# Performance work log

Measured on AMD Instinct MI355X. Metric: run time of the kernel, lower is better.

Reference implementation:

```python
import jax, jax.numpy as jnp
import numpy as np

THRESH = 1.0
TAU_M = 20.0
TAU_S = 5.0
NUM_STEPS = 8
SCALE = 0.2
BATCH = 8
DM = np.float32(np.exp(-1.0 / TAU_M))
DS = np.float32(np.exp(-1.0 / TAU_S))


@jax.custom_vjp
def spike_fn(x):
    return (x > 0.0).astype(x.dtype)

def _sf_fwd(x):
    return (x > 0.0).astype(x.dtype), x

def _sf_bwd(x, g):
    # rectangular surrogate gradient (lens = 0.5), standard for NOSO/SNN training
    return (g * (jnp.abs(x) < 0.5).astype(x.dtype),)

spike_fn.defvjp(_sf_fwd, _sf_bwd)


def conv5x5(x, w):
    return jax.lax.conv_general_dilated(x, w, (1, 1), ((2, 2), (2, 2)),
                                        dimension_numbers=('NCHW', 'OIHW', 'NCHW'))


def noso_conv(w, in_sp, sav, vm, vs):
    # dual-exponential NOSO neuron: pre-synaptic traces vm/vs, membrane u = sav*(conv(vm)-conv(vs))
    vm = DM * vm + in_sp
    vs = DS * vs + in_sp
    um = conv5x5(vm, w)
    us = conv5x5(vs, w)
    u = sav * (um - us)
    sp = spike_fn(u - THRESH)
    sav = sav * (1.0 - sp)  # one spike per neuron
    return sav, vm, vs, um, u, sp


def noso_fc(w, in_sp, sav, vm, vs):
    vm = DM * vm + in_sp
    vs = DS * vs + in_sp
    um = jnp.einsum('bi,oi->bo', vm, w)
    us = jnp.einsum('bi,oi->bo', vs, w)
    u = sav * (um - us)
    sp = spike_fn(u - THRESH)
    sav = sav * (1.0 - sp)
    return sav, vm, vs, um, u, sp


def minpool(sp, lat):
    # latency-based 2x2 min-pool: pass through the spike whose neuron fired earliest
    b, c, h, w = sp.shape
    s = sp.reshape(b, c, h // 2, 2, w // 2, 2).transpose(0, 1, 2, 4, 3, 5).reshape(b, c, h // 2, w // 2, 4)
    l = lat.reshape(b, c, h // 2, 2, w // 2, 2).transpose(0, 1, 2, 4, 3, 5).reshape(b, c, h // 2, w // 2, 4)
    idx = jnp.argmin(l, axis=-1)
    return jnp.take_along_axis(s, idx[..., None], axis=-1)[..., 0]


def xavier(key, shape, fan_in, fan_out):
    a = np.float32(np.sqrt(6.0 / (fan_in + fan_out)))
    return jax.random.uniform(key, shape, jnp.float32, -a, a)


def setup_inputs():
    key = jax.random.key(0)
    ks = jax.random.split(key, 9)
    inp = {'input': jax.random.uniform(ks[0], (BATCH, 3, 32, 32), jnp.float32)}
    def cw(k, o, i):
        return xavier(k, (o, i, 5, 5), i * 25, o * 25)
    def lw(k, o, i):
        return xavier(k, (o, i), i, o)
    inp['wc1'] = cw(ks[1], 64, 3)
    inp['wc2'] = cw(ks[2], 128, 64)
    inp['wc3'] = cw(ks[3], 256, 128)
    inp['wc4'] = cw(ks[4], 512, 256)
    inp['wc5'] = cw(ks[5], 256, 512)
    inp['wf1'] = lw(ks[6], 1024, 16384)
    inp['wf2'] = lw(ks[7], 512, 1024)
    inp['wf3'] = lw(ks[8], 10, 512)
    inp['batch_size'] = BATCH
    return inp


def forward(input, wc1, wc2, wc3, wc4, wc5, wf1, wf2, wf3, batch_size):
    B = batch_size
    f32 = jnp.float32
    def Z(*s):
        return jnp.zeros((B,) + s, f32)
    def O(*s):
        return jnp.ones((B,) + s, f32)
    carry = {
        'in_u': Z(3, 32, 32),
        'h1': (O(64, 32, 32), Z(3, 32, 32), Z(3, 32, 32)),
        'h2': (O(128, 32, 32), Z(64, 32, 32), Z(64, 32, 32)),
        'h3': (O(256, 16, 16), Z(128, 16, 16), Z(128, 16, 16)),
        'h4': (O(512, 8, 8), Z(256, 8, 8), Z(256, 8, 8)),
        'h5': (O(256, 8, 8), Z(512, 8, 8), Z(512, 8, 8)),
        'f1': (O(1024), Z(16384), Z(16384)),
        'f2': (O(512), Z(1024), Z(1024)),
        'f3': (O(10), Z(512), Z(512)),
        'p1e': Z(128, 32, 32),
        'p1l': float(NUM_STEPS) * O(128, 32, 32),
        'p2e': Z(256, 16, 16),
        'p2l': float(NUM_STEPS) * O(256, 16, 16),
        'te': Z(10),
        'out_t': float(NUM_STEPS) * O(10),
        'out_u': Z(10),
        'sum_sp': jnp.zeros((9,), f32),
    }

    def step(c, _):
        # input encoding neuron (thresh=1, leaky integrate + reset on spike)
        in_u = DM * c['in_u'] + input * SCALE
        in_sp = spike_fn(in_u - 1.0)
        in_u = in_u * (1.0 - in_sp)
        s1, vm1, vs1, um1, u1, sp1 = noso_conv(wc1, in_sp, *c['h1'])
        s2, vm2, vs2, um2, u2, sp2 = noso_conv(wc2, sp1, *c['h2'])
        p1e = c['p1e'] + ((c['p1e'] + (um2 != 0).astype(f32)) != 0).astype(f32)
        p1l = c['p1l'] + jax.lax.stop_gradient(sp2) * (p1e - NUM_STEPS + 1.0)
        s3, vm3, vs3, um3, u3, sp3 = noso_conv(wc3, minpool(sp2, p1l), *c['h3'])
        p2e = c['p2e'] + ((c['p2e'] + (um3 != 0).astype(f32)) != 0).astype(f32)
        p2l = c['p2l'] + jax.lax.stop_gradient(sp3) * (p2e - NUM_STEPS + 1.0)
        s4, vm4, vs4, um4, u4, sp4 = noso_conv(wc4, minpool(sp3, p2l), *c['h4'])
        s5, vm5, vs5, um5, u5, sp5 = noso_conv(wc5, sp4, *c['h5'])
        sf1, vmf1, vsf1, umf1, uf1, spf1 = noso_fc(wf1, sp5.reshape(B, -1), *c['f1'])
        sf2, vmf2, vsf2, umf2, uf2, spf2 = noso_fc(wf2, spf1, *c['f2'])
        sf3, vmf3, vsf3, umf3, uf3, spf3 = noso_fc(wf3, spf2, *c['f3'])
        te = c['te'] + ((c['te'] + (uf3 != 0).astype(f32)) != 0).astype(f32)
        out_t = c['out_t'] + spf3 * jax.lax.stop_gradient(te - NUM_STEPS)  # dodt forward
        out_u = c['out_u'] + spf3 * uf3
        sum_sp = c['sum_sp'] + jnp.stack([in_sp.sum(), sp1.sum(), sp2.sum(), sp3.sum(),
                                          sp4.sum(), sp5.sum(), spf1.sum(), spf2.sum(), spf3.sum()])
        nc = {'in_u': in_u,
              'h1': (s1, vm1, vs1), 'h2': (s2, vm2, vs2), 'h3': (s3, vm3, vs3),
              'h4': (s4, vm4, vs4), 'h5': (s5, vm5, vs5),
              'f1': (sf1, vmf1, vsf1), 'f2': (sf2, vmf2, vsf2), 'f3': (sf3, vmf3, vsf3),
              'p1e': p1e, 'p1l': p1l, 'p2e': p2e, 'p2l': p2l,
              'te': te, 'out_t': out_t, 'out_u': out_u, 'sum_sp': sum_sp}
        return nc, None

    c, _ = jax.lax.scan(step, carry, None, length=NUM_STEPS)
    return c['out_t'], c['out_u'], c['sum_sp']


def reference(input, wc1, wc2, wc3, wc4, wc5, wf1, wf2, wf3, batch_size):
    return forward(input, wc1, wc2, wc3, wc4, wc5, wf1, wf2, wf3, batch_size)
```

## Files before the change

kernel.cpp:

```cpp
#include <hip/hip_runtime.h>
#include <cstddef>

#define B 8
constexpr int TAIL_NB = 256;

constexpr float DM = 0.95122942450071400910f;
constexpr float DS = 0.81873075307798185867f;

constexpr int BS_L0 = 3 * 32 * 32;
constexpr int BS_L1 = 64 * 32 * 32;
constexpr int BS_P1 = 128 * 16 * 16;
constexpr int BS_P2 = 256 * 8 * 8;
constexpr int BS_L4 = 512 * 8 * 8;
constexpr int BS_L5 = 256 * 8 * 8;
constexpr int BS_F1 = 1024;
constexpr int BS_F2 = 512;

constexpr size_t I_L0 = 0;
constexpr size_t I_L1 = I_L0 + 8 * (size_t)B * BS_L0;
constexpr size_t I_P1 = I_L1 + 8 * (size_t)B * BS_L1;
constexpr size_t I_P2 = I_P1 + 8 * (size_t)B * BS_P1;
constexpr size_t I_L4 = I_P2 + 8 * (size_t)B * BS_P2;
constexpr size_t I_L5 = I_L4 + 8 * (size_t)B * BS_L4;
constexpr size_t I_F1 = I_L5 + 8 * (size_t)B * BS_L5;
constexpr size_t I_F2 = I_F1 + 8 * (size_t)B * BS_F1;
constexpr size_t I_CNT = I_F2 + 8 * (size_t)B * BS_F2;
constexpr size_t I_SUMP = I_CNT + 512;
constexpr size_t I_BAR = I_SUMP + 16;
constexpr size_t INT_TOTAL = I_BAR + 2;
constexpr size_t WS_NEED = INT_TOTAL * sizeof(int);

constexpr int ilog2(int n) { int l = 0; while (n > 1) { n >>= 1; ++l; } return l; }

__device__ __forceinline__ int ldcnt(const int* p) {
  return __hip_atomic_load(p, __ATOMIC_RELAXED, __HIP_MEMORY_SCOPE_AGENT);
}

__device__ __forceinline__ void block_stage(bool sp, int idx, int* s_list, int* s_n) {
  unsigned long long bal = __ballot(sp);
  if (bal == 0ull) return;
  int lane = threadIdx.x & 63;
  int leader = (int)__ffsll((unsigned long long)bal) - 1;
  int base = 0;
  if (lane == leader) base = atomicAdd(s_n, __popcll(bal));
  base = __shfl(base, leader);
  if (sp) s_list[base + __popcll(bal & ((1ull << lane) - 1ull))] = idx;
}

__device__ __forceinline__ void wave_append(bool sp, int idx, int* cnt, int* list) {
  unsigned long long bal = __ballot(sp);
  if (bal == 0ull) return;
  int lane = threadIdx.x & 63;
  int leader = (int)__ffsll((unsigned long long)bal) - 1;
  int base = 0;
  if (lane == leader) base = atomicAdd(cnt, __popcll(bal));
  base = __shfl(base, leader);
  if (sp) list[base + __popcll(bal & ((1ull << lane) - 1ull))] = idx;
}

__device__ __forceinline__ bool layer_any(const int* cnt, int ci, int tid, int* s_gate) {
  __syncthreads();
  if (tid == 0) *s_gate = 0;
  __syncthreads();
  if (tid < 64) {
    int t = tid >> 3, b = tid & 7;
    if (ldcnt(cnt + (t * 8 + ci) * 8 + b) > 0) *s_gate = 1;
  }
  __syncthreads();
  return *s_gate != 0;
}

__device__ __forceinline__ void gbar(int* bar, int tid) {
  __threadfence();
  __syncthreads();
  if (tid == 0) {
    int g = __hip_atomic_load(bar + 1, __ATOMIC_RELAXED, __HIP_MEMORY_SCOPE_AGENT);
    int a = __hip_atomic_fetch_add(bar, 1, __ATOMIC_ACQ_REL, __HIP_MEMORY_SCOPE_AGENT);
    if (a == TAIL_NB - 1) {
      __hip_atomic_store(bar, 0, __ATOMIC_RELAXED, __HIP_MEMORY_SCOPE_AGENT);
      __hip_atomic_store(bar + 1, g + 1, __ATOMIC_RELEASE, __HIP_MEMORY_SCOPE_AGENT);
    } else {
      while (__hip_atomic_load(bar + 1, __ATOMIC_ACQUIRE, __HIP_MEMORY_SCOPE_AGENT) == g)
        __builtin_amdgcn_s_sleep(1);
    }
  }
  __syncthreads();
  __threadfence();
}

__global__ __launch_bounds__(512) void k_encode(const float* __restrict__ in,
                                                int* __restrict__ iws) {
  const int tid = threadIdx.x;
  const int b = blockIdx.x;
  int* cnt = iws + I_CNT;
  if (tid < 56) {
    int t = tid / 7, ci = 1 + tid % 7;
    cnt[(t * 8 + ci) * 8 + b] = 0;
  }
  if (b == 0 && tid >= 64 && tid < 82) iws[I_SUMP + (tid - 64)] = 0;
  __shared__ unsigned long long s_bal[8 * 48];
  __shared__ int s_off[8 * 48];
  const int lane = tid & 63, w = tid >> 6;
  float x[6], u[6];
#pragma unroll
  for (int k = 0; k < 6; ++k) {
    x[k] = in[b * BS_L0 + tid + k * 512] * 0.2f;
    u[k] = 0.0f;
  }
  unsigned long long spmall = 0ull;
#pragma clang loop unroll(disable)
  for (int t = 0; t < 8; ++t) {
#pragma unroll
    for (int k = 0; k < 6; ++k) {
      u[k] = DM * u[k] + x[k];
      bool sp = (u[k] - 1.0f > 0.0f);
      if (sp) { u[k] = 0.0f; spmall |= 1ull << (t * 6 + k); }
      unsigned long long bal = __ballot(sp);
      if (lane == 0) s_bal[t * 48 + k * 8 + w] = bal;
    }
  }
  __syncthreads();
  if (lane < 48) {
    const int t = w;
    int v = __popcll(s_bal[t * 48 + lane]);
    int incl = v;
#pragma unroll
    for (int d = 1; d < 64; d <<= 1) {
      int o = __shfl_up(incl, d);
      if (lane >= d) incl += o;
    }
    s_off[t * 48 + lane] = incl - v;
    if (lane == 47) cnt[(t * 8 + 0) * 8 + b] = incl;
  }
  __syncthreads();
#pragma clang loop unroll(disable)
  for (int t = 0; t < 8; ++t) {
    int* list = iws + I_L0 + ((size_t)t * B + b) * BS_L0;
#pragma unroll
    for (int k = 0; k < 6; ++k) {
      if (spmall & (1ull << (t * 6 + k))) {
        int word = k * 8 + w;
        int rank = __popcll(s_bal[t * 48 + word] & ((1ull << lane) - 1ull));
        list[s_off[t * 48 + word] + rank] = tid + k * 512;
      }
    }
  }
}

__global__ __launch_bounds__(1024) void k_conv1(const float* __restrict__ w,
                                                int* __restrict__ iws) {
  const int tid = threadIdx.x;
  const int plane = blockIdx.x;
  const int b = plane >> 6;
  const int oc = plane & 63;
  int* cnt = iws + I_CNT;
  __shared__ float s_acc[8 * 1024];
  __shared__ float s_w[75];
  __shared__ int s_cnt[8];
  if (tid < 8) s_cnt[tid] = ldcnt(cnt + (tid * 8 + 0) * 8 + b);
  if (tid >= 64 && tid < 139) s_w[tid - 64] = w[oc * 75 + (tid - 64)];
#pragma unroll
  for (int t = 0; t < 8; ++t) s_acc[t * 1024 + tid] = 0.0f;
  __syncthreads();
#pragma clang loop unroll(disable)
  for (int t = 0; t < 8; ++t) {
    const int S = s_cnt[t];
    if (S == 0) continue;
    const int* glist = iws + I_L0 + ((size_t)t * B + b) * BS_L0;
    const int total = S << 5;
#pragma clang loop unroll(disable)
    for (int i = tid; i < total; i += 1024) {
      int k = i & 31;
      if (k < 25) {
        int loc = glist[i >> 5];
        int c = loc >> 10;
        int p = loc & 1023;
        int ki = (k * 205) >> 10;
        int oy = (p >> 5) + 2 - ki;
        int ox = (p & 31) + 2 - (k - ki * 5);
        if ((unsigned)oy < 32u && (unsigned)ox < 32u)
          atomicAdd(&s_acc[t * 1024 + (oy << 5) + ox], s_w[c * 25 + k]);
      }
    }
  }
  __syncthreads();
  float um = 0.0f, us = 0.0f, sav = 1.0f;
#pragma clang loop unroll(disable)
  for (int t = 0; t < 8; ++t) {
    float cv = s_acc[t * 1024 + tid];
    float m = DM * um + cv;
    float s2 = DS * us + cv;
    um = m;
    us = s2;
    float uu = sav * (m - s2);
    bool sp = (uu - 1.0f > 0.0f);
    if (sp) sav = 0.0f;
    wave_append(sp, (oc << 10) + tid, cnt + (t * 8 + 1) * 8 + b,
                iws + I_L1 + ((size_t)t * B + b) * BS_L1);
  }
}

template <int CIN, int COUT, int H, int W, bool POOL, int PPB, bool WLDS>
__device__ void conv_phase(int bid, int tid, const float* __restrict__ w, int* cnt, int in_ci,
                           int out_ci, const int* __restrict__ in_list0, int in_bs,
                           int* __restrict__ out_list0, int out_bs, float* sump_layer,
                           float* s_acc, float* s_plb, float* s_spb, float* s_w, int* s_list,
                           int* s_n, int* s_base, int* s_uc, int* s_cnt) {
  constexpr int HW = H * W;
  constexpr int HWlog = ilog2(HW);
  constexpr int Wlog = ilog2(W);
  constexpr int PPT = (HW + 255) / 256;
  int wcount = 0;
  const int b = (bid * PPB) >> ilog2(COUT);
  if (tid < 8) s_cnt[tid] = ldcnt(cnt + (tid * 8 + in_ci) * 8 + b);
  __syncthreads();
#pragma clang loop unroll(disable)
  for (int pl = 0; pl < PPB; ++pl) {
    const int plane = bid * PPB + pl;
    const int oc = plane & (COUT - 1);
    if constexpr (WLDS) {
#pragma clang loop unroll(disable)
      for (int j = tid; j < CIN * 25; j += 256) s_w[j] = w[(size_t)oc * CIN * 25 + j];
    }
    float um[PPT], us[PPT], sav[PPT], pe[PPT], plat[PPT];
#pragma unroll
    for (int k = 0; k < PPT; ++k) {
      um[k] = 0.0f; us[k] = 0.0f; sav[k] = 1.0f; pe[k] = 0.0f; plat[k] = 8.0f;
    }
    bool active = false;
#pragma clang loop unroll(disable)
    for (int t = 0; t < 8; ++t) {
      const int S = s_cnt[t];
      if (!active && S == 0) continue;
      active = true;
#pragma clang loop unroll(disable)
      for (int p = tid; p < HW; p += 256) s_acc[p] = 0.0f;
      if (tid == 0) *s_n = 0;
      __syncthreads();
      const int* list = in_list0 + ((size_t)t * B + b) * in_bs;
#pragma clang loop unroll(disable)
      for (int s = tid; s < S; s += 256) {
        int loc = list[s];
        int c = loc >> HWlog;
        int p = loc & (HW - 1);
        int y = p >> Wlog, x = p & (W - 1);
        const float* wp = WLDS ? (const float*)s_w + c * 25 : w + ((size_t)oc * CIN + c) * 25;
#pragma clang loop unroll(disable)
        for (int ki = 0; ki < 5; ++ki) {
          int oy = y + 2 - ki;
          if ((unsigned)oy < (unsigned)H) {
#pragma clang loop unroll(disable)
            for (int kj = 0; kj < 5; ++kj) {
              int ox = x + 2 - kj;
              if ((unsigned)ox < (unsigned)W) atomicAdd(&s_acc[oy * W + ox], wp[ki * 5 + kj]);
            }
          }
        }
      }
      __syncthreads();
#pragma unroll
      for (int k = 0; k < PPT; ++k) {
        int p = tid + k * 256;
        bool lane_ok = (p < HW);
        float cv = lane_ok ? s_acc[p] : 0.0f;
        float m = DM * um[k] + cv;
        float s2 = DS * us[k] + cv;
        um[k] = m;
        us[k] = s2;
        float uu = sav[k] * (m - s2);
        bool sp = lane_ok && (uu - 1.0f > 0.0f);
        if (sp) sav[k] = 0.0f;
        if constexpr (POOL) {
          unsigned long long bal = __ballot(sp);
          if ((tid & 63) == 0) wcount += (int)__popcll(bal);
          if (lane_ok) {
            float act = (m != 0.0f) ? 1.0f : 0.0f;
            float pen = pe[k] + (((pe[k] + act) != 0.0f) ? 1.0f : 0.0f);
            pe[k] = pen;
            if (sp) plat[k] += pen - 7.0f;
            s_plb[p] = plat[k];
            s_spb[p] = sp ? 1.0f : 0.0f;
          }
        } else {
          block_stage(sp, (oc << HWlog) + p, s_list, s_n);
        }
      }
      __syncthreads();
      if constexpr (POOL) {
        constexpr int HP = H / 2, WP = W / 2;
#pragma clang loop unroll(disable)
        for (int q = tid; q < HP * WP; q += 256) {
          int py = q / WP, px = q - py * WP;
          int base = (2 * py) * W + 2 * px;
          float l0 = s_plb[base], l1 = s_plb[base + 1], l2 = s_plb[base + W],
                l3 = s_plb[base + W + 1];
          int off = 0;
          float lm = l0;
          if (l1 < lm) { lm = l1; off = 1; }
          if (l2 < lm) { lm = l2; off = W; }
          if (l3 < lm) { lm = l3; off = W + 1; }
          bool psp = (s_spb[base + off] != 0.0f);
          block_stage(psp, oc * (HP * WP) + q, s_list, s_n);
        }
        __syncthreads();
      }
      if (tid == 0 && *s_n > 0) *s_base = atomicAdd(cnt + (t * 8 + out_ci) * 8 + b, *s_n);
      __syncthreads();
      int* out_list = out_list0 + ((size_t)t * B + b) * out_bs;
      int n = *s_n;
#pragma clang loop unroll(disable)
      for (int j = tid; j < n; j += 256) out_list[*s_base + j] = s_list[j];
      __syncthreads();
    }
  }
  if constexpr (POOL) {
    if (tid == 0) *s_uc = 0;
    __syncthreads();
    if ((tid & 63) == 0 && wcount) atomicAdd(s_uc, wcount);
    __syncthreads();
    if (tid == 0 && *s_uc) atomicAdd(sump_layer + b, (float)*s_uc);
  }
}

template <int IN, int OUT>
__device__ void fc_phase(int bid, int tid, const float* __restrict__ w, int* cnt, int in_ci,
                         int out_ci, const int* __restrict__ in_list0, int in_bs,
                         int* __restrict__ out_list0, int out_bs, int* s_list, int* s_n,
                         int* s_base, int* s_cnt) {
  const int q = bid * 256 + tid;
  const int b = q >> ilog2(OUT);
  const int o = q & (OUT - 1);
  if (tid < 8) s_cnt[tid] = ldcnt(cnt + (tid * 8 + in_ci) * 8 + b);
  __syncthreads();
  float um = 0.0f, us = 0.0f, sav = 1.0f;
  bool active = false;
#pragma clang loop unroll(disable)
  for (int t = 0; t < 8; ++t) {
    const int S = s_cnt[t];
    if (!active && S == 0) continue;
    active = true;
    if (tid == 0) *s_n = 0;
    __syncthreads();
    const int* list = in_list0 + ((size_t)t * B + b) * in_bs;
    float acc = 0.0f;
#pragma clang loop unroll(disable)
    for (int s = 0; s < S; ++s) acc += w[(size_t)o * IN + list[s]];
    float m = DM * um + acc;
    float s2 = DS * us + acc;
    um = m;
    us = s2;
    float uu = sav * (m - s2);
    bool sp = (uu - 1.0f > 0.0f);
    if (sp) sav = 0.0f;
    block_stage(sp, o, s_list, s_n);
    __syncthreads();
    if (tid == 0 && *s_n > 0) *s_base = atomicAdd(cnt + (t * 8 + out_ci) * 8 + b, *s_n);
    __syncthreads();
    int* out_list = out_list0 + ((size_t)t * B + b) * out_bs;
    int n = *s_n;
#pragma clang loop unroll(disable)
    for (int j = tid; j < n; j += 256) out_list[*s_base + j] = s_list[j];
    __syncthreads();
  }
}

__device__ void fc3_phase(int tid, const float* __restrict__ w, const int* cnt, int in_ci,
                          const int* __restrict__ in_list0, int in_bs,
                          const float* __restrict__ sump, float* __restrict__ out, int* s_c3) {
  if (tid == 0) *s_c3 = 0;
  __syncthreads();
  const bool lane_ok = (tid < 80);
  const int b = lane_ok ? tid / 10 : 0;
  const int o = lane_ok ? tid - b * 10 : 0;
  float um = 0.0f, us = 0.0f, sav = 1.0f, te = 0.0f, ot = 8.0f, ou = 0.0f;
  bool active = false;
#pragma clang loop unroll(disable)
  for (int t = 0; t < 8; ++t) {
    const int S = lane_ok ? ldcnt(cnt + (t * 8 + in_ci) * 8 + b) : 0;
    if (!active && !__any(S > 0)) continue;
    active = true;
    const int* list = in_list0 + ((size_t)t * B + b) * in_bs;
    float acc = 0.0f;
#pragma clang loop unroll(disable)
    for (int s = 0; s < S; ++s) acc += w[o * 512 + list[s]];
    float m = DM * um + acc;
    float s2 = DS * us + acc;
    um = m;
    us = s2;
    float uu = sav * (m - s2);
    bool sp = lane_ok && (uu - 1.0f > 0.0f);
    if (sp) sav = 0.0f;
    float act = (uu != 0.0f) ? 1.0f : 0.0f;
    te = te + (((te + act) != 0.0f) ? 1.0f : 0.0f);
    if (sp) {
      ot += te - 8.0f;
      ou += uu;
    }
    unsigned long long bal = __ballot(sp);
    if ((tid & 63) == 0 && bal) atomicAdd(s_c3, (int)__popcll(bal));
  }
  if (tid < 80) {
    out[tid] = ot;
    out[80 + tid] = ou;
  }
  __syncthreads();
  if (tid < 8) {
    float s = 0.0f;
    if (tid == 2 || tid == 3) {
      const float* sp = sump + (tid - 2) * 8;
      for (int b2 = 0; b2 < 8; ++b2) s += sp[b2];
    } else {
      for (int t = 0; t < 8; ++t)
        for (int b2 = 0; b2 < 8; ++b2) s += (float)cnt[(t * 8 + tid) * 8 + b2];
    }
    out[160 + tid] = s;
  }
  if (tid == 0) out[168] = (float)*s_c3;
}

__global__ __launch_bounds__(256) void k_tail(const float* __restrict__ wc2,
                                              const float* __restrict__ wc3,
                                              const float* __restrict__ wc4,
                                              const float* __restrict__ wc5,
                                              const float* __restrict__ wf1,
                                              const float* __restrict__ wf2,
                                              const float* __restrict__ wf3,
                                              float* __restrict__ out, int* __restrict__ iws) {
  __shared__ float s_w[3200];
  __shared__ float s_acc[1024];
  __shared__ float s_plb[1024];
  __shared__ float s_spb[1024];
  __shared__ int s_list[1024];
  __shared__ int s_n, s_base, s_uc, s_gate, s_c3, s_cnt[8];
  const int tid = threadIdx.x;
  const int bid = blockIdx.x;
  int* cnt = iws + I_CNT;
  float* sump = (float*)(iws + I_SUMP);
  int* bar = iws + I_BAR;

  if (layer_any(cnt, 1, tid, &s_gate)) {
    conv_phase<64, 128, 32, 32, true, 4, true>(bid, tid, wc2, cnt, 1, 2, iws + I_L1, BS_L1,
                                               iws + I_P1, BS_P1, sump + 0, s_acc, s_plb, s_spb,
                                               s_w, s_list, &s_n, &s_base, &s_uc, s_cnt);
    gbar(bar, tid);
  }
  if (layer_any(cnt, 2, tid, &s_gate)) {
    conv_phase<128, 256, 16, 16, true, 8, true>(bid, tid, wc3, cnt, 2, 3, iws + I_P1, BS_P1,
                                                iws + I_P2, BS_P2, sump + 8, s_acc, s_plb, s_spb,
                                                s_w, s_list, &s_n, &s_base, &s_uc, s_cnt);
    gbar(bar, tid);
  }
  if (layer_any(cnt, 3, tid, &s_gate)) {
    conv_phase<256, 512, 8, 8, false, 16, false>(bid, tid, wc4, cnt, 3, 4, iws + I_P2, BS_P2,
                                                 iws + I_L4, BS_L4, nullptr, s_acc, s_plb, s_spb,
                                                 s_w, s_list, &s_n, &s_base, &s_uc, s_cnt);
    gbar(bar, tid);
  }
  if (layer_any(cnt, 4, tid, &s_gate)) {
    conv_phase<512, 256, 8, 8, false, 8, false>(bid, tid, wc5, cnt, 4, 5, iws + I_L4, BS_L4,
                                                iws + I_L5, BS_L5, nullptr, s_acc, s_plb, s_spb,
                                                s_w, s_list, &s_n, &s_base, &s_uc, s_cnt);
    gbar(bar, tid);
  }
  if (layer_any(cnt, 5, tid, &s_gate)) {
    if (bid < B * 1024 / 256)
      fc_phase<16384, 1024>(bid, tid, wf1, cnt, 5, 6, iws + I_L5, BS_L5, iws + I_F1, BS_F1,
                            s_list, &s_n, &s_base, s_cnt);
    gbar(bar, tid);
  }
  if (layer_any(cnt, 6, tid, &s_gate)) {
    if (bid < B * 512 / 256)
      fc_phase<1024, 512>(bid, tid, wf2, cnt, 6, 7, iws + I_F1, BS_F1, iws + I_F2, BS_F2,
                          s_list, &s_n, &s_base, s_cnt);
    gbar(bar, tid);
  }
  if (bid == 0)
    fc3_phase(tid, wf3, cnt, 7, iws + I_F2, BS_F2, sump, out, &s_c3);
}

extern "C" void kernel_launch(void* const* d_in, const int* in_sizes, int n_in, void* d_out,
                              int out_size, void* d_ws, size_t ws_size, hipStream_t stream) {
  const float* input = (const float*)d_in[0];
  const float* wc1 = (const float*)d_in[1];
  const float* wc2 = (const float*)d_in[2];
  const float* wc3 = (const float*)d_in[3];
  const float* wc4 = (const float*)d_in[4];
  const float* wc5 = (const float*)d_in[5];
  const float* wf1 = (const float*)d_in[6];
  const float* wf2 = (const float*)d_in[7];
  const float* wf3 = (const float*)d_in[8];
  float* out = (float*)d_out;
  int* iws = (int*)d_ws;
  if (ws_size < WS_NEED) return;

  k_encode<<<B, 512, 0, stream>>>(input, iws);
  k_conv1<<<512, 1024, 0, stream>>>(wc1, iws);
  k_tail<<<TAIL_NB, 256, 0, stream>>>(wc2, wc3, wc4, wc5, wf1, wf2, wf3, out, iws);
}
```

Measured before the change: 67.69 us.

## Fold conv1 into persistent tail kernel and precompute all layer gates

```diff
diff --git a/kernel.cpp b/kernel.cpp
--- a/kernel.cpp
+++ b/kernel.cpp
@@ -70,6 +70,14 @@
   return *s_gate != 0;
 }
 
+__device__ __forceinline__ void all_gates(const int* cnt, int tid, int* s_any) {
+  if (tid < 8) s_any[tid] = 0;
+  __syncthreads();
+  for (int i = tid; i < 512; i += 256)
+    if (ldcnt(cnt + i) > 0) atomicOr(&s_any[(i >> 3) & 7], 1);
+  __syncthreads();
+}
+
 __device__ __forceinline__ void gbar(int* bar, int tid) {
   __threadfence();
   __syncthreads();
@@ -147,56 +155,62 @@
   }
 }
 
-__global__ __launch_bounds__(1024) void k_conv1(const float* __restrict__ w,
-                                                int* __restrict__ iws) {
-  const int tid = threadIdx.x;
-  const int plane = blockIdx.x;
-  const int b = plane >> 6;
-  const int oc = plane & 63;
-  int* cnt = iws + I_CNT;
-  __shared__ float s_acc[8 * 1024];
-  __shared__ float s_w[75];
-  __shared__ int s_cnt[8];
-  if (tid < 8) s_cnt[tid] = ldcnt(cnt + (tid * 8 + 0) * 8 + b);
-  if (tid >= 64 && tid < 139) s_w[tid - 64] = w[oc * 75 + (tid - 64)];
-#pragma unroll
-  for (int t = 0; t < 8; ++t) s_acc[t * 1024 + tid] = 0.0f;
-  __syncthreads();
-#pragma clang loop unroll(disable)
-  for (int t = 0; t < 8; ++t) {
-    const int S = s_cnt[t];
-    if (S == 0) continue;
-    const int* glist = iws + I_L0 + ((size_t)t * B + b) * BS_L0;
-    const int total = S << 5;
-#pragma clang loop unroll(disable)
-    for (int i = tid; i < total; i += 1024) {
-      int k = i & 31;
-      if (k < 25) {
-        int loc = glist[i >> 5];
-        int c = loc >> 10;
-        int p = loc & 1023;
-        int ki = (k * 205) >> 10;
-        int oy = (p >> 5) + 2 - ki;
-        int ox = (p & 31) + 2 - (k - ki * 5);
-        if ((unsigned)oy < 32u && (unsigned)ox < 32u)
-          atomicAdd(&s_acc[t * 1024 + (oy << 5) + ox], s_w[c * 25 + k]);
+__device__ void conv1_phase(int bid, int tid, const float* __restrict__ w, int* cnt,
+                            int* __restrict__ iws, float* s_big, float* s_w1, int* s_cnt) {
+#pragma clang loop unroll(disable)
+  for (int pl = 0; pl < 2; ++pl) {
+    const int plane = bid * 2 + pl;
+    const int b = plane >> 6;
+    const int oc = plane & 63;
+    if (tid < 8) s_cnt[tid] = ldcnt(cnt + (tid * 8 + 0) * 8 + b);
+    if (tid >= 64 && tid < 139) s_w1[tid - 64] = w[oc * 75 + (tid - 64)];
+#pragma clang loop unroll(disable)
+    for (int i = tid; i < 8192; i += 256) s_big[i] = 0.0f;
+    __syncthreads();
+#pragma clang loop unroll(disable)
+    for (int t = 0; t < 8; ++t) {
+      const int S = s_cnt[t];
+      if (S == 0) continue;
+      const int* glist = iws + I_L0 + ((size_t)t * B + b) * BS_L0;
+      const int total = S << 5;
+#pragma clang loop unroll(disable)
+      for (int i = tid; i < total; i += 256) {
+        int k = i & 31;
+        if (k < 25) {
+          int loc = glist[i >> 5];
+          int c = loc >> 10;
+          int p = loc & 1023;
+          int ki = (k * 205) >> 10;
+          int oy = (p >> 5) + 2 - ki;
+          int ox = (p & 31) + 2 - (k - ki * 5);
+          if ((unsigned)oy < 32u && (unsigned)ox < 32u)
+            atomicAdd(&s_big[t * 1024 + (oy << 5) + ox], s_w1[c * 25 + k]);
+        }
       }
     }
-  }
-  __syncthreads();
-  float um = 0.0f, us = 0.0f, sav = 1.0f;
-#pragma clang loop unroll(disable)
-  for (int t = 0; t < 8; ++t) {
-    float cv = s_acc[t * 1024 + tid];
-    float m = DM * um + cv;
-    float s2 = DS * us + cv;
-    um = m;
-    us = s2;
-    float uu = sav * (m - s2);
-    bool sp = (uu - 1.0f > 0.0f);
-    if (sp) sav = 0.0f;
-    wave_append(sp, (oc << 10) + tid, cnt + (t * 8 + 1) * 8 + b,
-                iws + I_L1 + ((size_t)t * B + b) * BS_L1);
+    __syncthreads();
+    float um[4], us4[4], sav[4];
+#pragma unroll
+    for (int k = 0; k < 4; ++k) { um[k] = 0.0f; us4[k] = 0.0f; sav[k] = 1.0f; }
+#pragma clang loop unroll(disable)
+    for (int t = 0; t < 8; ++t) {
+      int* out_cnt = cnt + (t * 8 + 1) * 8 + b;
+      int* out_list = iws + I_L1 + ((size_t)t * B + b) * BS_L1;
+#pragma unroll
+      for (int k = 0; k < 4; ++k) {
+        int p = tid + (k << 8);
+        float cv = s_big[t * 1024 + p];
+        float m = DM * um[k] + cv;
+        float s2 = DS * us4[k] + cv;
+        um[k] = m;
+        us4[k] = s2;
+        float uu = sav[k] * (m - s2);
+        bool sp = (uu - 1.0f > 0.0f);
+        if (sp) sav[k] = 0.0f;
+        wave_append(sp, (oc << 10) + p, out_cnt, out_list);
+      }
+    }
+    __syncthreads();
   }
 }
 
@@ -418,7 +432,8 @@
   if (tid == 0) out[168] = (float)*s_c3;
 }
 
-__global__ __launch_bounds__(256) void k_tail(const float* __restrict__ wc2,
+__global__ __launch_bounds__(256) void k_tail(const float* __restrict__ wc1,
+                                              const float* __restrict__ wc2,
                                               const float* __restrict__ wc3,
                                               const float* __restrict__ wc4,
                                               const float* __restrict__ wc5,
@@ -426,49 +441,64 @@
                                               const float* __restrict__ wf2,
                                               const float* __restrict__ wf3,
                                               float* __restrict__ out, int* __restrict__ iws) {
-  __shared__ float s_w[3200];
+  __shared__ float s_big[8192];
   __shared__ float s_acc[1024];
   __shared__ float s_plb[1024];
   __shared__ float s_spb[1024];
   __shared__ int s_list[1024];
-  __shared__ int s_n, s_base, s_uc, s_gate, s_c3, s_cnt[8];
+  __shared__ float s_w1[75];
+  __shared__ int s_n, s_base, s_uc, s_gate, s_c3, s_cnt[8], s_any[8];
   const int tid = threadIdx.x;
   const int bid = blockIdx.x;
   int* cnt = iws + I_CNT;
   float* sump = (float*)(iws + I_SUMP);
   int* bar = iws + I_BAR;
 
-  if (layer_any(cnt, 1, tid, &s_gate)) {
+  all_gates(cnt, tid, s_any);
+  bool g0 = s_any[0] != 0, g1 = s_any[1] != 0, g2 = s_any[2] != 0, g3 = s_any[3] != 0;
+  bool g4 = s_any[4] != 0, g5 = s_any[5] != 0, g6 = s_any[6] != 0;
+
+  if (g0) {
+    conv1_phase(bid, tid, wc1, cnt, iws, s_big, s_w1, s_cnt);
+    gbar(bar, tid);
+    g1 = layer_any(cnt, 1, tid, &s_gate);
+  }
+  if (g1) {
     conv_phase<64, 128, 32, 32, true, 4, true>(bid, tid, wc2, cnt, 1, 2, iws + I_L1, BS_L1,
                                                iws + I_P1, BS_P1, sump + 0, s_acc, s_plb, s_spb,
-                                               s_w, s_list, &s_n, &s_base, &s_uc, s_cnt);
-    gbar(bar, tid);
-  }
-  if (layer_any(cnt, 2, tid, &s_gate)) {
+                                               s_big, s_list, &s_n, &s_base, &s_uc, s_cnt);
+    gbar(bar, tid);
+    g2 = layer_any(cnt, 2, tid, &s_gate);
+  }
+  if (g2) {
     conv_phase<128, 256, 16, 16, true, 8, true>(bid, tid, wc3, cnt, 2, 3, iws + I_P1, BS_P1,
                                                 iws + I_P2, BS_P2, sump + 8, s_acc, s_plb, s_spb,
-                                                s_w, s_list, &s_n, &s_base, &s_uc, s_cnt);
-    gbar(bar, tid);
-  }
-  if (layer_any(cnt, 3, tid, &s_gate)) {
+                                                s_big, s_list, &s_n, &s_base, &s_uc, s_cnt);
+    gbar(bar, tid);
+    g3 = layer_any(cnt, 3, tid, &s_gate);
+  }
+  if (g3) {
     conv_phase<256, 512, 8, 8, false, 16, false>(bid, tid, wc4, cnt, 3, 4, iws + I_P2, BS_P2,
                                                  iws + I_L4, BS_L4, nullptr, s_acc, s_plb, s_spb,
-                                                 s_w, s_list, &s_n, &s_base, &s_uc, s_cnt);
-    gbar(bar, tid);
-  }
-  if (layer_any(cnt, 4, tid, &s_gate)) {
+                                                 s_big, s_list, &s_n, &s_base, &s_uc, s_cnt);
+    gbar(bar, tid);
+    g4 = layer_any(cnt, 4, tid, &s_gate);
+  }
+  if (g4) {
     conv_phase<512, 256, 8, 8, false, 8, false>(bid, tid, wc5, cnt, 4, 5, iws + I_L4, BS_L4,
                                                 iws + I_L5, BS_L5, nullptr, s_acc, s_plb, s_spb,
-                                                s_w, s_list, &s_n, &s_base, &s_uc, s_cnt);
-    gbar(bar, tid);
-  }
-  if (layer_any(cnt, 5, tid, &s_gate)) {
+                                                s_big, s_list, &s_n, &s_base, &s_uc, s_cnt);
+    gbar(bar, tid);
+    g5 = layer_any(cnt, 5, tid, &s_gate);
+  }
+  if (g5) {
     if (bid < B * 1024 / 256)
       fc_phase<16384, 1024>(bid, tid, wf1, cnt, 5, 6, iws + I_L5, BS_L5, iws + I_F1, BS_F1,
                             s_list, &s_n, &s_base, s_cnt);
     gbar(bar, tid);
-  }
-  if (layer_any(cnt, 6, tid, &s_gate)) {
+    g6 = layer_any(cnt, 6, tid, &s_gate);
+  }
+  if (g6) {
     if (bid < B * 512 / 256)
       fc_phase<1024, 512>(bid, tid, wf2, cnt, 6, 7, iws + I_F1, BS_F1, iws + I_F2, BS_F2,
                           s_list, &s_n, &s_base, s_cnt);
@@ -494,6 +524,5 @@
   if (ws_size < WS_NEED) return;
 
   k_encode<<<B, 512, 0, stream>>>(input, iws);
-  k_conv1<<<512, 1024, 0, stream>>>(wc1, iws);
-  k_tail<<<TAIL_NB, 256, 0, stream>>>(wc2, wc3, wc4, wc5, wf1, wf2, wf3, out, iws);
-}
+  k_tail<<<TAIL_NB, 256, 0, stream>>>(wc1, wc2, wc3, wc4, wc5, wf1, wf2, wf3, out, iws);
+}
```

Result: slower. 133.7 us (+97.5%).
